# Kernel optimization log

Hardware: AMD Instinct MI355X
Metric: run time of the kernel (lower is better)

Reference implementation:

```python
import jax, jax.numpy as jnp
import numpy as np

B, T, I, H, O = 8192, 128, 28, 200, 10


def setup_inputs() -> dict:
    key = jax.random.key(0)
    ks = jax.random.split(key, 7)
    s_ih = 1.0 / np.sqrt(H)
    return {
        "x": jax.random.normal(ks[0], (B, T, I), dtype=jnp.float32),
        "W_ih": jax.random.uniform(ks[1], (H, I), jnp.float32, -s_ih, s_ih),
        "W_hh": jax.random.uniform(ks[2], (H, H), jnp.float32, -s_ih, s_ih),
        "b_ih": jax.random.uniform(ks[3], (H,), jnp.float32, -s_ih, s_ih),
        "b_hh": jax.random.uniform(ks[4], (H,), jnp.float32, -s_ih, s_ih),
        "W_fc": jax.random.uniform(ks[5], (O, H), jnp.float32, -s_ih, s_ih),
        "b_fc": jax.random.uniform(ks[6], (O,), jnp.float32, -s_ih, s_ih),
    }


def reference(x, W_ih, W_hh, b_ih, b_hh, W_fc, b_fc):
    # Precompute input projections for all timesteps in one GEMM: [B,T,H]
    xp = jnp.einsum("bti,hi->bth", x, W_ih) + b_ih + b_hh
    h0 = jnp.zeros((x.shape[0], W_hh.shape[0]), dtype=x.dtype)

    def step(h, xp_t):
        # h_t = relu(x_t W_ih^T + b_ih + h_{t-1} W_hh^T + b_hh)
        h = jax.nn.relu(xp_t + h @ W_hh.T)
        return h, None

    # scan over time: xp transposed to [T,B,H]
    h_last, _ = jax.lax.scan(step, h0, jnp.swapaxes(xp, 0, 1))
    # out[:, -1, :] then fc1
    return h_last @ W_fc.T + b_fc
```

## Files before the change

### kernel.cpp

```cpp
#include <hip/hip_runtime.h>

typedef float f4v __attribute__((ext_vector_type(4)));
typedef short s8v __attribute__((ext_vector_type(8)));

#define TT 128
#define II 28
#define HH 200
#define BB 16
#define NT 256
#define SH 232
#define KX 224
#define SF 212

__device__ __forceinline__ short f2bf(float f) {
    union { float f; unsigned u; } a; a.f = f;
    unsigned r = a.u + 0x7FFFu + ((a.u >> 16) & 1u);
    return (short)(r >> 16);
}

__global__ __launch_bounds__(NT, 2)
void rnn_mfma2(const float* __restrict__ x,
               const float* __restrict__ W_ih,
               const float* __restrict__ W_hh,
               const float* __restrict__ b_ih,
               const float* __restrict__ b_hh,
               const float* __restrict__ W_fc,
               const float* __restrict__ b_fc,
               float* __restrict__ out)
{
    __shared__ __align__(16) short Hs[2][BB][SH];
    __shared__ __align__(16) float Hf[BB][SF];

    const int tid  = threadIdx.x;
    const int lane = tid & 63;
    const int q    = lane >> 4;
    const int lr   = lane & 15;
    const int wave = tid >> 6;
    const int b0   = blockIdx.x * BB;

    const int first = (wave == 0) ? 0 : 1 + 3 * wave;
    const int cnt   = (wave == 0) ? 4 : 3;

    for (int i = tid; i < 2 * BB * SH / 2; i += NT) ((int*)Hs)[i] = 0;

    s8v Af[4][8];
    #pragma unroll
    for (int u = 0; u < 4; ++u) {
        const int j = 16 * (first + u) + lr;
        #pragma unroll
        for (int kc = 0; kc < 8; ++kc) {
            const int k0 = 32 * kc + 8 * q;
            union { short s[8]; s8v v; } tv;
            #pragma unroll
            for (int i = 0; i < 8; ++i) {
                const int k = k0 + i;
                float w = 0.0f;
                if (u < cnt && j < HH) {
                    if (k < HH)                     w = W_hh[j * HH + k];
                    else if (k >= KX && k < KX+II)  w = W_ih[j * II + (k - KX)];
                }
                tv.s[i] = f2bf(w);
            }
            Af[u][kc] = tv.v;
        }
    }

    f4v biasv[4];
    #pragma unroll
    for (int u = 0; u < 4; ++u) {
        const int jt = first + u;
        f4v bv = {0.f, 0.f, 0.f, 0.f};
        #pragma unroll
        for (int i = 0; i < 4; ++i) {
            const int j = 16 * jt + 4 * q + i;
            if (u < cnt && j < HH) bv[i] = b_ih[j] + b_hh[j];
        }
        biasv[u] = bv;
    }

    const float* xp = x + (long)(b0 + lr) * TT * II + 8 * q;
    f4v xa0 = {0,0,0,0}, xb0 = {0,0,0,0}, xa1 = {0,0,0,0}, xb1 = {0,0,0,0};
    xa0 = *(const f4v*)(xp);
    if (q != 3) xb0 = *(const f4v*)(xp + 4);
    xa1 = *(const f4v*)(xp + II);
    if (q != 3) xb1 = *(const f4v*)(xp + II + 4);

    __syncthreads();

    auto step = [&](int t, int pb, f4v& xa, f4v& xb) {
        union { short s[8]; s8v v; } xf;
        #pragma unroll
        for (int i = 0; i < 4; ++i) { xf.s[i] = f2bf(xa[i]); xf.s[4+i] = f2bf(xb[i]); }
        {
            const int tn = (t + 2 < TT) ? t + 2 : TT - 1;
            xa = *(const f4v*)(xp + tn * II);
            if (q != 3) xb = *(const f4v*)(xp + tn * II + 4);
        }

        f4v acc[4];
        #pragma unroll
        for (int u = 0; u < 4; ++u) acc[u] = biasv[u];

        #pragma unroll
        for (int kc = 0; kc < 7; ++kc) {
            const s8v bf = *(const s8v*)&Hs[pb][lr][32 * kc + 8 * q];
            #pragma unroll
            for (int u = 0; u < 4; ++u)
                if (u < cnt)
                    acc[u] = __builtin_amdgcn_mfma_f32_16x16x32_bf16(Af[u][kc], bf, acc[u], 0, 0, 0);
        }
        #pragma unroll
        for (int u = 0; u < 4; ++u)
            if (u < cnt)
                acc[u] = __builtin_amdgcn_mfma_f32_16x16x32_bf16(Af[u][7], xf.v, acc[u], 0, 0, 0);

        #pragma unroll
        for (int u = 0; u < 4; ++u) {
            if (u < cnt) {
                const int jt = first + u;
                const f4v a = acc[u];
                const float r0 = fmaxf(a.x, 0.f), r1 = fmaxf(a.y, 0.f);
                const float r2 = fmaxf(a.z, 0.f), r3 = fmaxf(a.w, 0.f);
                short4 hv;
                hv.x = f2bf(r0); hv.y = f2bf(r1); hv.z = f2bf(r2); hv.w = f2bf(r3);
                *(short4*)&Hs[pb ^ 1][lr][16 * jt + 4 * q] = hv;
                if (t == TT - 1) {
                    f4v rf = {r0, r1, r2, r3};
                    *(f4v*)&Hf[lr][16 * jt + 4 * q] = rf;
                }
            }
        }
        __syncthreads();
    };

    for (int tb = 0; tb < TT; tb += 2) {
        step(tb,     0, xa0, xb0);
        step(tb + 1, 1, xa1, xb1);
    }

    if (tid < BB * 10) {
        const int o = tid >> 4, r = tid & 15;
        float s = b_fc[o];
        for (int k = 0; k < HH; ++k)
            s = fmaf(Hf[r][k], W_fc[o * HH + k], s);
        __builtin_nontemporal_store(s, &out[(b0 + r) * 10 + o]);
    }
}

extern "C" void kernel_launch(void* const* d_in, const int* in_sizes, int n_in,
                              void* d_out, int out_size, void* d_ws, size_t ws_size,
                              hipStream_t stream) {
    const float* x    = (const float*)d_in[0];
    const float* W_ih = (const float*)d_in[1];
    const float* W_hh = (const float*)d_in[2];
    const float* b_ih = (const float*)d_in[3];
    const float* b_hh = (const float*)d_in[4];
    const float* W_fc = (const float*)d_in[5];
    const float* b_fc = (const float*)d_in[6];
    float* out = (float*)d_out;

    rnn_mfma2<<<dim3(8192 / BB), dim3(NT), 0, stream>>>(
        x, W_ih, W_hh, b_ih, b_hh, W_fc, b_fc, out);
}
```

Before: 318.5 us.

## Split hidden tiles across two waves per block instead of four

Each block now runs two waves, and each wave owns up to seven 16-row hidden tiles. That keeps 56 bf16 weight fragments per lane in registers and hoists all h-state LDS reads ahead of the MFMA chains. Fewer waves means the per-step barrier synchronises less, and each wave's reads of the shared h state are reused across more tiles. The bf16 conversion also switches to packed hardware intrinsics. In exchange, register pressure rises sharply (launch bounds of 1) and each step has fewer waves to hide MFMA dependency latency, which may hurt occupancy.

```diff
diff --git a/kernel.cpp b/kernel.cpp
--- a/kernel.cpp
+++ b/kernel.cpp
@@ -1,4 +1,5 @@
 #include <hip/hip_runtime.h>
+#include <hip/hip_bf16.h>
 
 typedef float f4v __attribute__((ext_vector_type(4)));
 typedef short s8v __attribute__((ext_vector_type(8)));
@@ -7,26 +8,31 @@
 #define II 28
 #define HH 200
 #define BB 16
-#define NT 256
+#define NT 128
 #define SH 232
 #define KX 224
 #define SF 212
 
+__device__ __forceinline__ int pk_bf16(float a, float b) {
+    union { __hip_bfloat162 h; int i; } u;
+    u.h = __float22bfloat162_rn(make_float2(a, b));
+    return u.i;
+}
 __device__ __forceinline__ short f2bf(float f) {
-    union { float f; unsigned u; } a; a.f = f;
-    unsigned r = a.u + 0x7FFFu + ((a.u >> 16) & 1u);
-    return (short)(r >> 16);
+    union { __hip_bfloat16 h; short s; } u;
+    u.h = __float2bfloat16(f);
+    return u.s;
 }
 
-__global__ __launch_bounds__(NT, 2)
-void rnn_mfma2(const float* __restrict__ x,
-               const float* __restrict__ W_ih,
-               const float* __restrict__ W_hh,
-               const float* __restrict__ b_ih,
-               const float* __restrict__ b_hh,
-               const float* __restrict__ W_fc,
-               const float* __restrict__ b_fc,
-               float* __restrict__ out)
+__global__ __launch_bounds__(NT, 1)
+void rnn_w2(const float* __restrict__ x,
+            const float* __restrict__ W_ih,
+            const float* __restrict__ W_hh,
+            const float* __restrict__ b_ih,
+            const float* __restrict__ b_hh,
+            const float* __restrict__ W_fc,
+            const float* __restrict__ b_fc,
+            float* __restrict__ out)
 {
     __shared__ __align__(16) short Hs[2][BB][SH];
     __shared__ __align__(16) float Hf[BB][SF];
@@ -38,26 +44,25 @@
     const int wave = tid >> 6;
     const int b0   = blockIdx.x * BB;
 
-    const int first = (wave == 0) ? 0 : 1 + 3 * wave;
-    const int cnt   = (wave == 0) ? 4 : 3;
+    const int first = wave * 7;
+    const int cnt   = wave ? 6 : 7;
 
     for (int i = tid; i < 2 * BB * SH / 2; i += NT) ((int*)Hs)[i] = 0;
 
-    s8v Af[4][8];
+    s8v Af[7][8];
     #pragma unroll
-    for (int u = 0; u < 4; ++u) {
+    for (int u = 0; u < 7; ++u) {
         const int j = 16 * (first + u) + lr;
         #pragma unroll
         for (int kc = 0; kc < 8; ++kc) {
-            const int k0 = 32 * kc + 8 * q;
             union { short s[8]; s8v v; } tv;
             #pragma unroll
             for (int i = 0; i < 8; ++i) {
-                const int k = k0 + i;
+                const int k = 32 * kc + 8 * q + i;
                 float w = 0.0f;
                 if (u < cnt && j < HH) {
-                    if (k < HH)                     w = W_hh[j * HH + k];
-                    else if (k >= KX && k < KX+II)  w = W_ih[j * II + (k - KX)];
+                    if (k < HH)                    w = W_hh[j * HH + k];
+                    else if (k >= KX && k < KX+II) w = W_ih[j * II + (k - KX)];
                 }
                 tv.s[i] = f2bf(w);
             }
@@ -65,20 +70,19 @@
         }
     }
 
-    f4v biasv[4];
+    f4v biasv[7];
     #pragma unroll
-    for (int u = 0; u < 4; ++u) {
-        const int jt = first + u;
+    for (int u = 0; u < 7; ++u) {
         f4v bv = {0.f, 0.f, 0.f, 0.f};
         #pragma unroll
         for (int i = 0; i < 4; ++i) {
-            const int j = 16 * jt + 4 * q + i;
+            const int j = 16 * (first + u) + 4 * q + i;
             if (u < cnt && j < HH) bv[i] = b_ih[j] + b_hh[j];
         }
         biasv[u] = bv;
     }
 
-    const float* xp = x + (long)(b0 + lr) * TT * II + 8 * q;
+    const float* xp = x + (long)(b0 + lr) * (TT * II) + 8 * q;
     f4v xa0 = {0,0,0,0}, xb0 = {0,0,0,0}, xa1 = {0,0,0,0}, xb1 = {0,0,0,0};
     xa0 = *(const f4v*)(xp);
     if (q != 3) xb0 = *(const f4v*)(xp + 4);
@@ -88,42 +92,37 @@
     __syncthreads();
 
     auto step = [&](int t, int pb, f4v& xa, f4v& xb) {
-        union { short s[8]; s8v v; } xf;
-        #pragma unroll
-        for (int i = 0; i < 4; ++i) { xf.s[i] = f2bf(xa[i]); xf.s[4+i] = f2bf(xb[i]); }
+        union { int i4[4]; s8v v; } xf;
+        xf.i4[0] = pk_bf16(xa.x, xa.y);
+        xf.i4[1] = pk_bf16(xa.z, xa.w);
+        xf.i4[2] = pk_bf16(xb.x, xb.y);
+        xf.i4[3] = pk_bf16(xb.z, xb.w);
         {
             const int tn = (t + 2 < TT) ? t + 2 : TT - 1;
             xa = *(const f4v*)(xp + tn * II);
             if (q != 3) xb = *(const f4v*)(xp + tn * II + 4);
         }
 
-        f4v acc[4];
+        s8v bf[7];
         #pragma unroll
-        for (int u = 0; u < 4; ++u) acc[u] = biasv[u];
+        for (int kc = 0; kc < 7; ++kc)
+            bf[kc] = *(const s8v*)&Hs[pb][lr][32 * kc + 8 * q];
 
         #pragma unroll
-        for (int kc = 0; kc < 7; ++kc) {
-            const s8v bf = *(const s8v*)&Hs[pb][lr][32 * kc + 8 * q];
-            #pragma unroll
-            for (int u = 0; u < 4; ++u)
-                if (u < cnt)
-                    acc[u] = __builtin_amdgcn_mfma_f32_16x16x32_bf16(Af[u][kc], bf, acc[u], 0, 0, 0);
-        }
-        #pragma unroll
-        for (int u = 0; u < 4; ++u)
-            if (u < cnt)
-                acc[u] = __builtin_amdgcn_mfma_f32_16x16x32_bf16(Af[u][7], xf.v, acc[u], 0, 0, 0);
-
-        #pragma unroll
-        for (int u = 0; u < 4; ++u) {
+        for (int u = 0; u < 7; ++u) {
             if (u < cnt) {
                 const int jt = first + u;
-                const f4v a = acc[u];
-                const float r0 = fmaxf(a.x, 0.f), r1 = fmaxf(a.y, 0.f);
-                const float r2 = fmaxf(a.z, 0.f), r3 = fmaxf(a.w, 0.f);
-                short4 hv;
-                hv.x = f2bf(r0); hv.y = f2bf(r1); hv.z = f2bf(r2); hv.w = f2bf(r3);
-                *(short4*)&Hs[pb ^ 1][lr][16 * jt + 4 * q] = hv;
+                f4v acc = __builtin_amdgcn_mfma_f32_16x16x32_bf16(Af[u][7], xf.v, biasv[u], 0, 0, 0);
+                #pragma unroll
+                for (int kc = 0; kc < 7; ++kc)
+                    acc = __builtin_amdgcn_mfma_f32_16x16x32_bf16(Af[u][kc], bf[kc], acc, 0, 0, 0);
+
+                const float r0 = fmaxf(acc.x, 0.f), r1 = fmaxf(acc.y, 0.f);
+                const float r2 = fmaxf(acc.z, 0.f), r3 = fmaxf(acc.w, 0.f);
+                int2 hv;
+                hv.x = pk_bf16(r0, r1);
+                hv.y = pk_bf16(r2, r3);
+                *(int2*)&Hs[pb ^ 1][lr][16 * jt + 4 * q] = hv;
                 if (t == TT - 1) {
                     f4v rf = {r0, r1, r2, r3};
                     *(f4v*)&Hf[lr][16 * jt + 4 * q] = rf;
@@ -138,12 +137,12 @@
         step(tb + 1, 1, xa1, xb1);
     }
 
-    if (tid < BB * 10) {
-        const int o = tid >> 4, r = tid & 15;
+    for (int i = tid; i < BB * 10; i += NT) {
+        const int o = i >> 4, r = i & 15;
         float s = b_fc[o];
         for (int k = 0; k < HH; ++k)
             s = fmaf(Hf[r][k], W_fc[o * HH + k], s);
-        __builtin_nontemporal_store(s, &out[(b0 + r) * 10 + o]);
+        __builtin_nontemporal_store(s, &out[(long)(b0 + r) * 10 + o]);
     }
 }
 
@@ -159,6 +158,6 @@
     const float* b_fc = (const float*)d_in[6];
     float* out = (float*)d_out;
 
-    rnn_mfma2<<<dim3(8192 / BB), dim3(NT), 0, stream>>>(
+    rnn_w2<<<dim3(8192 / BB), dim3(NT), 0, stream>>>(
         x, W_ih, W_hh, b_ih, b_hh, W_fc, b_fc, out);
 }
```

New measurement: 325.4 us. 2.2% more time.

## Stage x chunks into LDS asynchronously and cheapen bf16 conversion

Applied to the files above, without the earlier changes.

Replaces the per-step register prefetch of x with double-buffered chunks of 8 timesteps. Waves 2-3 copy them global-to-LDS with global_load_lds, so the recurrence reads x from shared memory. Float-to-bf16 packing changes from round-to-nearest-even to round-half-up, using a perm instruction to pack pairs. The input MFMA is moved first and the hidden-state fragments are loaded up front. The final fp32 hidden buffer is dropped and the FC layer reads the bf16 state instead, which saves LDS but loses some precision in the output. There is a race risk: the chunk copy is issued without an explicit wait before its buffer is read.

```diff
diff --git a/kernel.cpp b/kernel.cpp
--- a/kernel.cpp
+++ b/kernel.cpp
@@ -1,6 +1,7 @@
 #include <hip/hip_runtime.h>
 
 typedef float f4v __attribute__((ext_vector_type(4)));
+typedef float f2v __attribute__((ext_vector_type(2)));
 typedef short s8v __attribute__((ext_vector_type(8)));
 
 #define TT 128
@@ -10,26 +11,30 @@
 #define NT 256
 #define SH 232
 #define KX 224
-#define SF 212
+#define CH 8
+#define XW (CH * BB * II)
 
+__device__ __forceinline__ unsigned pk_hu(float a, float b) {
+    unsigned ua = __builtin_bit_cast(unsigned, a) + 0x8000u;
+    unsigned ub = __builtin_bit_cast(unsigned, b) + 0x8000u;
+    return __builtin_amdgcn_perm(ub, ua, 0x07060302);
+}
 __device__ __forceinline__ short f2bf(float f) {
-    union { float f; unsigned u; } a; a.f = f;
-    unsigned r = a.u + 0x7FFFu + ((a.u >> 16) & 1u);
-    return (short)(r >> 16);
+    return (short)((__builtin_bit_cast(unsigned, f) + 0x8000u) >> 16);
 }
 
 __global__ __launch_bounds__(NT, 2)
-void rnn_mfma2(const float* __restrict__ x,
-               const float* __restrict__ W_ih,
-               const float* __restrict__ W_hh,
-               const float* __restrict__ b_ih,
-               const float* __restrict__ b_hh,
-               const float* __restrict__ W_fc,
-               const float* __restrict__ b_fc,
-               float* __restrict__ out)
+void rnn_r7(const float* __restrict__ x,
+            const float* __restrict__ W_ih,
+            const float* __restrict__ W_hh,
+            const float* __restrict__ b_ih,
+            const float* __restrict__ b_hh,
+            const float* __restrict__ W_fc,
+            const float* __restrict__ b_fc,
+            float* __restrict__ out)
 {
     __shared__ __align__(16) short Hs[2][BB][SH];
-    __shared__ __align__(16) float Hf[BB][SF];
+    __shared__ __align__(16) float Xl[2][XW + 8];
 
     const int tid  = threadIdx.x;
     const int lane = tid & 63;
@@ -49,15 +54,14 @@
         const int j = 16 * (first + u) + lr;
         #pragma unroll
         for (int kc = 0; kc < 8; ++kc) {
-            const int k0 = 32 * kc + 8 * q;
             union { short s[8]; s8v v; } tv;
             #pragma unroll
             for (int i = 0; i < 8; ++i) {
-                const int k = k0 + i;
+                const int k = 32 * kc + 8 * q + i;
                 float w = 0.0f;
                 if (u < cnt && j < HH) {
-                    if (k < HH)                     w = W_hh[j * HH + k];
-                    else if (k >= KX && k < KX+II)  w = W_ih[j * II + (k - KX)];
+                    if (k < HH)                    w = W_hh[j * HH + k];
+                    else if (k >= KX && k < KX+II) w = W_ih[j * II + (k - KX)];
                 }
                 tv.s[i] = f2bf(w);
             }
@@ -68,82 +72,106 @@
     f4v biasv[4];
     #pragma unroll
     for (int u = 0; u < 4; ++u) {
-        const int jt = first + u;
         f4v bv = {0.f, 0.f, 0.f, 0.f};
         #pragma unroll
         for (int i = 0; i < 4; ++i) {
-            const int j = 16 * jt + 4 * q + i;
+            const int j = 16 * (first + u) + 4 * q + i;
             if (u < cnt && j < HH) bv[i] = b_ih[j] + b_hh[j];
         }
         biasv[u] = bv;
     }
 
-    const float* xp = x + (long)(b0 + lr) * TT * II + 8 * q;
-    f4v xa0 = {0,0,0,0}, xb0 = {0,0,0,0}, xa1 = {0,0,0,0}, xb1 = {0,0,0,0};
-    xa0 = *(const f4v*)(xp);
-    if (q != 3) xb0 = *(const f4v*)(xp + 4);
-    xa1 = *(const f4v*)(xp + II);
-    if (q != 3) xb1 = *(const f4v*)(xp + II + 4);
+    const int wv = wave - 2;
+    long xoff[7];
+    #pragma unroll
+    for (int e = 0; e < 7; ++e) {
+        if (wv >= 0) {
+            const int m  = ((wv * 7 + e) << 6) + lane;
+            const int tl = m / 112;
+            const int rm = m - tl * 112;
+            const int r  = rm / 7;
+            const int c4 = rm - r * 7;
+            xoff[e] = ((long)(b0 + r) * TT + tl) * II + c4 * 4;
+        } else xoff[e] = 0;
+    }
+    auto load_chunk = [&](int cc) {
+        if (wv >= 0) {
+            float* dbase = &Xl[cc & 1][(wv * 7) * 256];
+            #pragma unroll
+            for (int e = 0; e < 7; ++e) {
+                const float* src = x + xoff[e] + (long)cc * (CH * II);
+                __builtin_amdgcn_global_load_lds(
+                    (const __attribute__((address_space(1))) void*)src,
+                    (__attribute__((address_space(3))) void*)(dbase + e * 256),
+                    16, 0, 0);
+            }
+        }
+    };
 
+    load_chunk(0);
     __syncthreads();
 
-    auto step = [&](int t, int pb, f4v& xa, f4v& xb) {
-        union { short s[8]; s8v v; } xf;
+    for (int c = 0; c < TT / CH; ++c) {
+        if (c + 1 < TT / CH) load_chunk(c + 1);
         #pragma unroll
-        for (int i = 0; i < 4; ++i) { xf.s[i] = f2bf(xa[i]); xf.s[4+i] = f2bf(xb[i]); }
-        {
-            const int tn = (t + 2 < TT) ? t + 2 : TT - 1;
-            xa = *(const f4v*)(xp + tn * II);
-            if (q != 3) xb = *(const f4v*)(xp + tn * II + 4);
-        }
+        for (int s = 0; s < CH; ++s) {
+            const int t  = c * CH + s;
+            const int pb = t & 1;
 
-        f4v acc[4];
-        #pragma unroll
-        for (int u = 0; u < 4; ++u) acc[u] = biasv[u];
+            s8v bf[7];
+            #pragma unroll
+            for (int kc = 0; kc < 7; ++kc)
+                bf[kc] = *(const s8v*)&Hs[pb][lr][32 * kc + 8 * q];
 
-        #pragma unroll
-        for (int kc = 0; kc < 7; ++kc) {
-            const s8v bf = *(const s8v*)&Hs[pb][lr][32 * kc + 8 * q];
+            const float* xr = &Xl[c & 1][s * (BB * II) + lr * II + 8 * q];
+            const f2v x0 = *(const f2v*)(xr + 0);
+            const f2v x1 = *(const f2v*)(xr + 2);
+            const f2v x2 = *(const f2v*)(xr + 4);
+            const f2v x3 = *(const f2v*)(xr + 6);
+            union { unsigned u4[4]; s8v v; } xf;
+            xf.u4[0] = pk_hu(x0.x, x0.y);
+            xf.u4[1] = pk_hu(x1.x, x1.y);
+            xf.u4[2] = pk_hu(x2.x, x2.y);
+            xf.u4[3] = pk_hu(x3.x, x3.y);
+
+            f4v acc[4];
             #pragma unroll
             for (int u = 0; u < 4; ++u)
                 if (u < cnt)
-                    acc[u] = __builtin_amdgcn_mfma_f32_16x16x32_bf16(Af[u][kc], bf, acc[u], 0, 0, 0);
-        }
-        #pragma unroll
-        for (int u = 0; u < 4; ++u)
-            if (u < cnt)
-                acc[u] = __builtin_amdgcn_mfma_f32_16x16x32_bf16(Af[u][7], xf.v, acc[u], 0, 0, 0);
+                    acc[u] = __builtin_amdgcn_mfma_f32_16x16x32_bf16(Af[u][7], xf.v, biasv[u], 0, 0, 0);
+            #pragma unroll
+            for (int kc = 0; kc < 7; ++kc) {
+                #pragma unroll
+                for (int u = 0; u < 4; ++u)
+                    if (u < cnt)
+                        acc[u] = __builtin_amdgcn_mfma_f32_16x16x32_bf16(Af[u][kc], bf[kc], acc[u], 0, 0, 0);
+            }
 
-        #pragma unroll
-        for (int u = 0; u < 4; ++u) {
-            if (u < cnt) {
-                const int jt = first + u;
-                const f4v a = acc[u];
-                const float r0 = fmaxf(a.x, 0.f), r1 = fmaxf(a.y, 0.f);
-                const float r2 = fmaxf(a.z, 0.f), r3 = fmaxf(a.w, 0.f);
-                short4 hv;
-                hv.x = f2bf(r0); hv.y = f2bf(r1); hv.z = f2bf(r2); hv.w = f2bf(r3);
-                *(short4*)&Hs[pb ^ 1][lr][16 * jt + 4 * q] = hv;
-                if (t == TT - 1) {
-                    f4v rf = {r0, r1, r2, r3};
-                    *(f4v*)&Hf[lr][16 * jt + 4 * q] = rf;
+            #pragma unroll
+            for (int u = 0; u < 4; ++u) {
+                if (u < cnt) {
+                    const int jt = first + u;
+                    const float r0 = fmaxf(acc[u].x, 0.f), r1 = fmaxf(acc[u].y, 0.f);
+                    const float r2 = fmaxf(acc[u].z, 0.f), r3 = fmaxf(acc[u].w, 0.f);
+                    int2 hv;
+                    hv.x = (int)pk_hu(r0, r1);
+                    hv.y = (int)pk_hu(r2, r3);
+                    *(int2*)&Hs[pb ^ 1][lr][16 * jt + 4 * q] = hv;
                 }
             }
+            __syncthreads();
         }
-        __syncthreads();
-    };
-
-    for (int tb = 0; tb < TT; tb += 2) {
-        step(tb,     0, xa0, xb0);
-        step(tb + 1, 1, xa1, xb1);
     }
 
     if (tid < BB * 10) {
         const int o = tid >> 4, r = tid & 15;
-        float s = b_fc[o];
-        for (int k = 0; k < HH; ++k)
-            s = fmaf(Hf[r][k], W_fc[o * HH + k], s);
-        __builtin_nontemporal_store(s, &out[(b0 + r) * 10 + o]);
+        float sacc = b_fc[o];
+        for (int k = 0; k < HH; ++k) {
+            const float hk = __builtin_bit_cast(float,
+                (unsigned)((unsigned short)Hs[0][r][k]) << 16);
+            sacc = fmaf(hk, W_fc[o * HH + k], sacc);
+        }
+        __builtin_nontemporal_store(sacc, &out[(long)(b0 + r) * 10 + o]);
     }
 }
 
@@ -159,6 +187,6 @@
     const float* b_fc = (const float*)d_in[6];
     float* out = (float*)d_out;
 
-    rnn_mfma2<<<dim3(8192 / BB), dim3(NT), 0, stream>>>(
+    rnn_r7<<<dim3(8192 / BB), dim3(NT), 0, stream>>>(
         x, W_ih, W_hh, b_ih, b_hh, W_fc, b_fc, out);
 }
```

Measured after the change: 302.3 us. 1.05x faster.
